# Performance work log

Hardware: AMD Instinct MI355X
Metric: run time of the kernel (lower is better)

The kernel has to match this reference:

```python
import jax, jax.numpy as jnp
import numpy as np

B, N, C = 16, 2048, 256  # dim=256, hidden_dim=2*dim -> v,gate each width C
LN_EPS = 1e-5


def setup_inputs() -> dict:
    key = jax.random.key(0)
    ks = jax.random.split(key, 6)
    std = 0.02
    return {
        "x": jax.random.normal(ks[0], (B, N, C), dtype=jnp.float32),
        "H": 64,
        "W": 32,
        "ln_w": jnp.ones((C,), jnp.float32),
        "ln_b": jnp.zeros((C,), jnp.float32),
        "w_hidden": jax.random.normal(ks[1], (C, 2 * C), jnp.float32) * std,
        "b_hidden": jnp.zeros((2 * C,), jnp.float32),
        "w_kv": jax.random.normal(ks[2], (C, C), jnp.float32) * std,  # qkv_bias=False
        "gamma": jnp.ones((2, C), jnp.float32),   # torch.ones(2, dim)
        "beta": jnp.zeros((2, C), jnp.float32),   # torch.zeros(2, dim)
        "w_proj": jax.random.normal(ks[3], (C, C), jnp.float32) * std,
        "b_proj": jnp.zeros((C,), jnp.float32),
    }


def reference(x, H, W, ln_w, ln_b, w_hidden, b_hidden, w_kv, gamma, beta, w_proj, b_proj):
    # H, W are unused by the original forward (pos conv is dead code).
    b, n, c = x.shape
    # LayerNorm
    mu = jnp.mean(x, axis=-1, keepdims=True)
    var = jnp.mean(jnp.square(x - mu), axis=-1, keepdims=True)
    normed = (x - mu) * jax.lax.rsqrt(var + LN_EPS) * ln_w + ln_b
    # to_hidden: Linear + SiLU, then chunk into v, gate (each width c)
    h = jax.nn.silu(normed @ w_hidden + b_hidden)
    v, gate = h[..., :c], h[..., c:]
    # kv projection, then offset-scale into q, k
    Z = normed @ w_kv                                  # (b, n, c)
    QK = Z[..., None, :] * gamma + beta                # (b, n, 2, c)
    q, k = QK[..., 0, :], QK[..., 1, :]
    # relu^2 quadratic attention (no softmax)
    attn = jnp.einsum('bid,bjd->bij', q, k) / n        # (b, n, n)
    A = jnp.square(jax.nn.relu(attn))
    V = jnp.einsum('bij,bjd->bid', A, v)               # (b, n, c)
    # SiLU gating, output projection, residual
    out = (V * gate) @ w_proj + b_proj
    return out + x
```

## Files before the change

### kernel.cpp

```cpp
#include <hip/hip_runtime.h>

#define BN 32768
#define NB 16
#define NN 2048
#define CC 256
#define JT 64
#define NTILES (NN / JT)

using short8  = __attribute__((ext_vector_type(8))) short;
using floatx4 = __attribute__((ext_vector_type(4))) float;

__device__ __forceinline__ unsigned short f2bf(float f) {
  unsigned u = __builtin_bit_cast(unsigned, f);
  u += 0x7fffu + ((u >> 16) & 1u);
  return (unsigned short)(u >> 16);
}
__device__ __forceinline__ float bf2f(unsigned short h) {
  unsigned u = ((unsigned)h) << 16;
  return __builtin_bit_cast(float, u);
}
__device__ __forceinline__ unsigned char f2fp8(float f) {
  return (unsigned char)(__builtin_amdgcn_cvt_pk_fp8_f32(f, f, 0, false) & 0xff);
}
__device__ __forceinline__ long lo64(uint4 v) {
  uint2 t; t.x = v.x; t.y = v.y; return __builtin_bit_cast(long, t);
}
__device__ __forceinline__ long hi64(uint4 v) {
  uint2 t; t.x = v.z; t.y = v.w; return __builtin_bit_cast(long, t);
}
__device__ __forceinline__ void gll16(const void* g, void* l) {
  __builtin_amdgcn_global_load_lds(
      (const __attribute__((address_space(1))) void*)g,
      (__attribute__((address_space(3))) void*)l, 16, 0, 0);
}

__global__ __launch_bounds__(256) void ln_kernel(
    const float* __restrict__ x, const float* __restrict__ lw,
    const float* __restrict__ lb, unsigned short* __restrict__ normed) {
  int row  = blockIdx.x * 4 + (threadIdx.x >> 6);
  int lane = threadIdx.x & 63;
  float4 v = ((const float4*)(x + (size_t)row * CC))[lane];
  float s  = v.x + v.y + v.z + v.w;
  float s2 = v.x * v.x + v.y * v.y + v.z * v.z + v.w * v.w;
#pragma unroll
  for (int off = 32; off; off >>= 1) {
    s  += __shfl_xor(s, off);
    s2 += __shfl_xor(s2, off);
  }
  float mu = s * (1.0f / CC);
  float rs = rsqrtf(s2 * (1.0f / CC) - mu * mu + 1e-5f);
  float4 w = ((const float4*)lw)[lane];
  float4 b = ((const float4*)lb)[lane];
  ushort4 o;
  o.x = f2bf((v.x - mu) * rs * w.x + b.x);
  o.y = f2bf((v.y - mu) * rs * w.y + b.y);
  o.z = f2bf((v.z - mu) * rs * w.z + b.z);
  o.w = f2bf((v.w - mu) * rs * w.w + b.w);
  ((ushort4*)(normed + (size_t)row * CC))[lane] = o;
}

__global__ void wconv_kernel(const float* __restrict__ wh,
                             const float* __restrict__ wkv,
                             const float* __restrict__ wp,
                             unsigned short* __restrict__ wTh,
                             unsigned short* __restrict__ wTkv,
                             unsigned short* __restrict__ wTp) {
  int idx = blockIdx.x * 256 + threadIdx.x;
  if (idx < 131072) {
    int n = idx >> 8, k = idx & 255;
    wTh[idx] = f2bf(wh[(size_t)k * 512 + n]);
  } else if (idx < 196608) {
    int i2 = idx - 131072;
    int n = i2 >> 8, k = i2 & 255;
    wTkv[i2] = f2bf(wkv[(size_t)k * 256 + n]);
  } else {
    int i2 = idx - 196608;
    int n = i2 >> 8, k = i2 & 255;
    wTp[i2] = f2bf(wp[(size_t)k * 256 + n]);
  }
}

__global__ __launch_bounds__(256) void gemm_hidden(
    const unsigned short* __restrict__ A, const unsigned short* __restrict__ BT,
    const float* __restrict__ bias,
    unsigned char* __restrict__ vB, unsigned short* __restrict__ gout) {
  int wave = threadIdx.x >> 6, lane = threadIdx.x & 63;
  int m = lane & 15, g4 = lane >> 4, kb = g4 * 8;
  int m0 = blockIdx.x * 128 + (wave & 1) * 64;
  int n0 = blockIdx.y * 128 + (wave >> 1) * 64;
  floatx4 acc[4][4] = {};
#pragma unroll
  for (int ks = 0; ks < 8; ++ks) {
    short8 af[4], bf[4];
#pragma unroll
    for (int i = 0; i < 4; ++i)
      af[i] = *(const short8*)(A + (size_t)(m0 + i * 16 + m) * CC + ks * 32 + kb);
#pragma unroll
    for (int j = 0; j < 4; ++j)
      bf[j] = *(const short8*)(BT + (size_t)(n0 + j * 16 + m) * CC + ks * 32 + kb);
#pragma unroll
    for (int i = 0; i < 4; ++i)
#pragma unroll
      for (int j = 0; j < 4; ++j)
        acc[i][j] = __builtin_amdgcn_mfma_f32_16x16x32_bf16(af[i], bf[j], acc[i][j], 0, 0, 0);
  }
  const size_t tb = ((size_t)(m0 >> 11) * 32 + ((m0 & 2047) >> 6)) * 16384;
#pragma unroll
  for (int j = 0; j < 4; ++j) {
    int col = n0 + j * 16 + m;
    float bv = bias[col];
    size_t colb = tb + (size_t)col * 64;
#pragma unroll
    for (int i = 0; i < 4; ++i) {
      int h8 = ((i >> 1) & 1) * 8;
      int i2 = i * 2;
#pragma unroll
      for (int r = 0; r < 4; ++r) {
        int row = m0 + i * 16 + g4 * 4 + r;
        float hh = acc[i][j][r] + bv;
        float sv = hh / (1.0f + __expf(-hh));
        if (col < CC) {
          int val = g4 * 4 + r;
          int g4a = (i2 + (val >> 3)) & 3;
          vB[colb + g4a * 16 + h8 + (val & 7)] = f2fp8(sv);
        } else {
          gout[(size_t)row * CC + col - CC] = f2bf(sv);
        }
      }
    }
  }
}

__global__ __launch_bounds__(256) void gemm_kv(
    const unsigned short* __restrict__ A, const unsigned short* __restrict__ BT,
    const float* __restrict__ gamma, const float* __restrict__ beta,
    unsigned char* __restrict__ qout, unsigned char* __restrict__ kout) {
  int wave = threadIdx.x >> 6, lane = threadIdx.x & 63;
  int m = lane & 15, g4 = lane >> 4, kb = g4 * 8;
  int m0 = blockIdx.x * 128 + (wave & 1) * 64;
  int n0 = blockIdx.y * 128 + (wave >> 1) * 64;
  floatx4 acc[4][4] = {};
#pragma unroll
  for (int ks = 0; ks < 8; ++ks) {
    short8 af[4], bf[4];
#pragma unroll
    for (int i = 0; i < 4; ++i)
      af[i] = *(const short8*)(A + (size_t)(m0 + i * 16 + m) * CC + ks * 32 + kb);
#pragma unroll
    for (int j = 0; j < 4; ++j)
      bf[j] = *(const short8*)(BT + (size_t)(n0 + j * 16 + m) * CC + ks * 32 + kb);
#pragma unroll
    for (int i = 0; i < 4; ++i)
#pragma unroll
      for (int j = 0; j < 4; ++j)
        acc[i][j] = __builtin_amdgcn_mfma_f32_16x16x32_bf16(af[i], bf[j], acc[i][j], 0, 0, 0);
  }
  const size_t base0 = ((size_t)(m0 >> 11) * 128 + ((m0 & 2047) >> 4)) * 4096;
  const int mm = g4 * 4;
#pragma unroll
  for (int j = 0; j < 4; ++j) {
    int col = n0 + j * 16 + m;
    float g0 = gamma[col], b0 = beta[col];
    float g1 = gamma[CC + col], b1 = beta[CC + col];
    int cbase = (col >> 6) * 1024 + ((col >> 3) & 3) * 16 + ((col >> 5) & 1) * 8 + (col & 7);
#pragma unroll
    for (int i = 0; i < 4; ++i) {
      size_t ibase = base0 + (size_t)i * 4096 + cbase;
#pragma unroll
      for (int r = 0; r < 4; ++r) {
        float z = acc[i][j][r];
        size_t addr = ibase + (size_t)(mm + r) * 64;
        qout[addr] = f2fp8(z * g0 + b0);
        kout[addr] = f2fp8(z * g1 + b1);
      }
    }
  }
}

__global__ __launch_bounds__(256, 2) void attn_kernel(
    const unsigned char* __restrict__ qB, const unsigned char* __restrict__ kB,
    const unsigned char* __restrict__ vB, const unsigned short* __restrict__ gg,
    unsigned short* __restrict__ og) {
  __shared__ unsigned char Kl[2][16384];
  __shared__ unsigned char Vl[2][16384];
  const int tid = threadIdx.x;
  const int wave = tid >> 6, lane = tid & 63;
  const int m = lane & 15, g4 = lane >> 4;
  const int id = blockIdx.x;
  const int b = id & 15, bx = id >> 4;
  const int i0 = bx * 64;
  const unsigned char* kimg = kB + (size_t)b * 524288;
  const unsigned char* vimg = vB + (size_t)b * 524288;

  const int iblk = bx * 4 + wave;
  uint4 qf[4];
#pragma unroll
  for (int ks2 = 0; ks2 < 4; ++ks2)
    qf[ks2] = *(const uint4*)(qB + ((size_t)(b * 128 + iblk) * 4 + ks2) * 1024 + m * 64 + g4 * 16);

  floatx4 acc[16] = {};
  const int alo = (m + ((g4 & 1) << 5)) << 2;
  const int ahi = alo + 64;

  auto stage = [&](int buf, int t) {
    const unsigned char* kt = kimg + (size_t)t * 16384;
    const unsigned char* vt = vimg + (size_t)t * 16384;
#pragma unroll
    for (int it = 0; it < 4; ++it) {
      int o = (it * 256 + tid) * 16;
      gll16(kt + o, &Kl[buf][o]);
      gll16(vt + o, &Vl[buf][o]);
    }
  };

  stage(0, 0);
  for (int t = 0; t < NTILES; ++t) {
    const int cur = t & 1;
    __syncthreads();
    if (t + 1 < NTILES) stage(cur ^ 1, t + 1);
    floatx4 sacc[4] = {};
#pragma unroll
    for (int ks2 = 0; ks2 < 4; ++ks2) {
#pragma unroll
      for (int jf = 0; jf < 4; ++jf) {
        uint4 kf = *(const uint4*)(&Kl[cur][(jf * 4 + ks2) * 1024 + m * 64 + g4 * 16]);
        sacc[jf] = __builtin_amdgcn_mfma_f32_16x16x32_fp8_fp8(
            lo64(kf), lo64(qf[ks2]), sacc[jf], 0, 0, 0);
        sacc[jf] = __builtin_amdgcn_mfma_f32_16x16x32_fp8_fp8(
            hi64(kf), hi64(qf[ks2]), sacc[jf], 0, 0, 0);
      }
    }
    unsigned pk[4];
#pragma unroll
    for (int jf = 0; jf < 4; ++jf) {
      float p0 = fmaxf(sacc[jf][0], 0.0f) * 0.0625f;
      float p1 = fmaxf(sacc[jf][1], 0.0f) * 0.0625f;
      float p2 = fmaxf(sacc[jf][2], 0.0f) * 0.0625f;
      float p3 = fmaxf(sacc[jf][3], 0.0f) * 0.0625f;
      unsigned u = __builtin_amdgcn_cvt_pk_fp8_f32(p2 * p2, p3 * p3, 0, true);
      pk[jf] = __builtin_amdgcn_cvt_pk_fp8_f32(p0 * p0, p1 * p1, (int)u, false);
    }
    long ap[2];
#pragma unroll
    for (int kk = 0; kk < 2; ++kk) {
      int A0 = __builtin_amdgcn_ds_bpermute(alo, (int)pk[2 * kk]);
      int B0 = __builtin_amdgcn_ds_bpermute(alo, (int)pk[2 * kk + 1]);
      int C0 = __builtin_amdgcn_ds_bpermute(ahi, (int)pk[2 * kk]);
      int D0 = __builtin_amdgcn_ds_bpermute(ahi, (int)pk[2 * kk + 1]);
      unsigned lo = (g4 & 2) ? (unsigned)B0 : (unsigned)A0;
      unsigned hi = (g4 & 2) ? (unsigned)D0 : (unsigned)C0;
      ap[kk] = (long)(((unsigned long long)hi << 32) | lo);
    }
#pragma unroll
    for (int cf = 0; cf < 16; ++cf) {
      uint4 vfr = *(const uint4*)(&Vl[cur][cf * 1024 + m * 64 + g4 * 16]);
      acc[cf] = __builtin_amdgcn_mfma_f32_16x16x32_fp8_fp8(ap[0], lo64(vfr), acc[cf], 0, 0, 0);
      acc[cf] = __builtin_amdgcn_mfma_f32_16x16x32_fp8_fp8(ap[1], hi64(vfr), acc[cf], 0, 0, 0);
    }
  }
  const float sc = 1.0f / 16384.0f;
  const size_t bo = (size_t)b * NN * CC;
#pragma unroll
  for (int cf = 0; cf < 16; ++cf)
#pragma unroll
    for (int r = 0; r < 4; ++r) {
      int row = i0 + wave * 16 + g4 * 4 + r;
      int col = cf * 16 + m;
      size_t off = bo + (size_t)row * CC + col;
      og[off] = f2bf(acc[cf][r] * sc * bf2f(gg[off]));
    }
}

__global__ __launch_bounds__(256) void gemm_proj(
    const unsigned short* __restrict__ A, const unsigned short* __restrict__ BT,
    const float* __restrict__ bias, const float* __restrict__ xres,
    float* __restrict__ out) {
  int wave = threadIdx.x >> 6, lane = threadIdx.x & 63;
  int m = lane & 15, g4 = lane >> 4, kb = g4 * 8;
  int m0 = blockIdx.x * 128 + (wave & 1) * 64;
  int n0 = blockIdx.y * 128 + (wave >> 1) * 64;
  floatx4 acc[4][4] = {};
#pragma unroll
  for (int ks = 0; ks < 8; ++ks) {
    short8 af[4], bf[4];
#pragma unroll
    for (int i = 0; i < 4; ++i)
      af[i] = *(const short8*)(A + (size_t)(m0 + i * 16 + m) * CC + ks * 32 + kb);
#pragma unroll
    for (int j = 0; j < 4; ++j)
      bf[j] = *(const short8*)(BT + (size_t)(n0 + j * 16 + m) * CC + ks * 32 + kb);
#pragma unroll
    for (int i = 0; i < 4; ++i)
#pragma unroll
      for (int j = 0; j < 4; ++j)
        acc[i][j] = __builtin_amdgcn_mfma_f32_16x16x32_bf16(af[i], bf[j], acc[i][j], 0, 0, 0);
  }
#pragma unroll
  for (int j = 0; j < 4; ++j) {
    int col = n0 + j * 16 + m;
    float bv = bias[col];
#pragma unroll
    for (int i = 0; i < 4; ++i)
#pragma unroll
      for (int r = 0; r < 4; ++r) {
        int row = m0 + i * 16 + g4 * 4 + r;
        size_t rr = (size_t)row * CC;
        out[rr + col] = acc[i][j][r] + bv + xres[rr + col];
      }
  }
}

extern "C" void kernel_launch(void* const* d_in, const int* in_sizes, int n_in,
                              void* d_out, int out_size, void* d_ws, size_t ws_size,
                              hipStream_t stream) {
  const float* x        = (const float*)d_in[0];
  const float* ln_w     = (const float*)d_in[3];
  const float* ln_b     = (const float*)d_in[4];
  const float* w_hidden = (const float*)d_in[5];
  const float* b_hidden = (const float*)d_in[6];
  const float* w_kv     = (const float*)d_in[7];
  const float* gamma    = (const float*)d_in[8];
  const float* beta     = (const float*)d_in[9];
  const float* w_proj   = (const float*)d_in[10];
  const float* b_proj   = (const float*)d_in[11];
  float* out = (float*)d_out;
  char* ws = (char*)d_ws;

  const size_t SZ = (size_t)BN * CC * 2;
  const size_t HZ = SZ / 2;
  unsigned short* slot0 = (unsigned short*)(ws);
  unsigned short* gbuf  = (unsigned short*)(ws + SZ);
  unsigned char*  qB    = (unsigned char*)(ws + 2 * SZ);
  unsigned char*  kB    = (unsigned char*)(ws + 2 * SZ + HZ);
  unsigned char*  vB    = (unsigned char*)(ws + 2 * SZ + 2 * HZ);
  unsigned short* wTh   = (unsigned short*)(ws + 2 * SZ + 3 * HZ);
  unsigned short* wTkv  = (unsigned short*)(ws + 2 * SZ + 3 * HZ + 512 * 256 * 2);
  unsigned short* wTp   = (unsigned short*)(ws + 2 * SZ + 3 * HZ + 512 * 256 * 2 + 256 * 256 * 2);

  wconv_kernel<<<1024, 256, 0, stream>>>(w_hidden, w_kv, w_proj, wTh, wTkv, wTp);
  ln_kernel<<<BN / 4, 256, 0, stream>>>(x, ln_w, ln_b, slot0);
  gemm_hidden<<<dim3(BN / 128, 4), 256, 0, stream>>>(slot0, wTh, b_hidden, vB, gbuf);
  gemm_kv<<<dim3(BN / 128, 2), 256, 0, stream>>>(slot0, wTkv, gamma, beta, qB, kB);
  attn_kernel<<<512, 256, 0, stream>>>(qB, kB, vB, gbuf, slot0);
  gemm_proj<<<dim3(BN / 128, 2), 256, 0, stream>>>(slot0, wTp, b_proj, x, out);
}
```

Baseline: 178.5 us.

## Swizzle K/V fp8 tile layout and pack fp8 stores in projection epilogues

```diff
diff --git a/kernel.cpp b/kernel.cpp
--- a/kernel.cpp
+++ b/kernel.cpp
@@ -21,6 +21,10 @@
 }
 __device__ __forceinline__ unsigned char f2fp8(float f) {
   return (unsigned char)(__builtin_amdgcn_cvt_pk_fp8_f32(f, f, 0, false) & 0xff);
+}
+__device__ __forceinline__ unsigned pk4fp8(float a, float b, float c, float d) {
+  unsigned u = __builtin_amdgcn_cvt_pk_fp8_f32(c, d, 0, true);
+  return __builtin_amdgcn_cvt_pk_fp8_f32(a, b, (int)u, false);
 }
 __device__ __forceinline__ long lo64(uint4 v) {
   uint2 t; t.x = v.x; t.y = v.y; return __builtin_bit_cast(long, t);
@@ -104,29 +108,43 @@
       for (int j = 0; j < 4; ++j)
         acc[i][j] = __builtin_amdgcn_mfma_f32_16x16x32_bf16(af[i], bf[j], acc[i][j], 0, 0, 0);
   }
-  const size_t tb = ((size_t)(m0 >> 11) * 32 + ((m0 & 2047) >> 6)) * 16384;
-#pragma unroll
-  for (int j = 0; j < 4; ++j) {
-    int col = n0 + j * 16 + m;
-    float bv = bias[col];
-    size_t colb = tb + (size_t)col * 64;
-#pragma unroll
-    for (int i = 0; i < 4; ++i) {
-      int h8 = ((i >> 1) & 1) * 8;
-      int i2 = i * 2;
-#pragma unroll
-      for (int r = 0; r < 4; ++r) {
-        int row = m0 + i * 16 + g4 * 4 + r;
-        float hh = acc[i][j][r] + bv;
-        float sv = hh / (1.0f + __expf(-hh));
-        if (col < CC) {
-          int val = g4 * 4 + r;
-          int g4a = (i2 + (val >> 3)) & 3;
-          vB[colb + g4a * 16 + h8 + (val & 7)] = f2fp8(sv);
-        } else {
+  const int sw = (m >> 1) & 3;
+  if (n0 < CC) {
+    const size_t tb = ((size_t)(m0 >> 11) * 32 + ((m0 & 2047) >> 6)) * 16384;
+    const int jp4 = (g4 & 1) * 4;
+    const int g4h = g4 >> 1;
+#pragma unroll
+    for (int j = 0; j < 4; ++j) {
+      int col = n0 + j * 16 + m;
+      float bv = bias[col];
+      size_t colb = tb + (size_t)col * 64;
+#pragma unroll
+      for (int i = 0; i < 4; ++i) {
+        int g4a = ((i * 2 + g4h) & 3) ^ sw;
+        int h8 = ((i >> 1) & 1) * 8;
+        float s[4];
+#pragma unroll
+        for (int r = 0; r < 4; ++r) {
+          float hh = acc[i][j][r] + bv;
+          s[r] = hh / (1.0f + __expf(-hh));
+        }
+        *(unsigned*)(vB + colb + g4a * 16 + h8 + jp4) = pk4fp8(s[0], s[1], s[2], s[3]);
+      }
+    }
+  } else {
+#pragma unroll
+    for (int j = 0; j < 4; ++j) {
+      int col = n0 + j * 16 + m;
+      float bv = bias[col];
+#pragma unroll
+      for (int i = 0; i < 4; ++i)
+#pragma unroll
+        for (int r = 0; r < 4; ++r) {
+          int row = m0 + i * 16 + g4 * 4 + r;
+          float hh = acc[i][j][r] + bv;
+          float sv = hh / (1.0f + __expf(-hh));
           gout[(size_t)row * CC + col - CC] = f2bf(sv);
         }
-      }
     }
   }
 }
@@ -153,26 +171,32 @@
     for (int i = 0; i < 4; ++i)
 #pragma unroll
       for (int j = 0; j < 4; ++j)
-        acc[i][j] = __builtin_amdgcn_mfma_f32_16x16x32_bf16(af[i], bf[j], acc[i][j], 0, 0, 0);
-  }
-  const size_t base0 = ((size_t)(m0 >> 11) * 128 + ((m0 & 2047) >> 4)) * 4096;
-  const int mm = g4 * 4;
+        acc[i][j] = __builtin_amdgcn_mfma_f32_16x16x32_bf16(bf[j], af[i], acc[i][j], 0, 0, 0);
+  }
+  const int sw = (m >> 1) & 3;
 #pragma unroll
   for (int j = 0; j < 4; ++j) {
-    int col = n0 + j * 16 + m;
-    float g0 = gamma[col], b0 = beta[col];
-    float g1 = gamma[CC + col], b1 = beta[CC + col];
-    int cbase = (col >> 6) * 1024 + ((col >> 3) & 3) * 16 + ((col >> 5) & 1) * 8 + (col & 7);
+    int c4 = n0 + j * 16 + g4 * 4;
+    float4 g0 = *(const float4*)(gamma + c4);
+    float4 b0 = *(const float4*)(beta + c4);
+    float4 g1 = *(const float4*)(gamma + CC + c4);
+    float4 b1 = *(const float4*)(beta + CC + c4);
+    int ks2 = c4 >> 6;
+    int hsub = ((c4 >> 5) & 1) * 8 + (c4 & 7);
+    int qsub = ((c4 >> 3) & 3) * 16 + hsub;
+    int ksub = ((((c4 >> 3) & 3) ^ sw)) * 16 + hsub;
 #pragma unroll
     for (int i = 0; i < 4; ++i) {
-      size_t ibase = base0 + (size_t)i * 4096 + cbase;
-#pragma unroll
-      for (int r = 0; r < 4; ++r) {
-        float z = acc[i][j][r];
-        size_t addr = ibase + (size_t)(mm + r) * 64;
-        qout[addr] = f2fp8(z * g0 + b0);
-        kout[addr] = f2fp8(z * g1 + b1);
-      }
+      int n = m0 + i * 16 + m;
+      int bb = n >> 11, jj = n & 2047;
+      size_t base = (((size_t)bb * 128 + (jj >> 4)) * 4 + ks2) * 1024 + (size_t)m * 64;
+      floatx4 z = acc[i][j];
+      unsigned qu = pk4fp8(z[0] * g0.x + b0.x, z[1] * g0.y + b0.y,
+                           z[2] * g0.z + b0.z, z[3] * g0.w + b0.w);
+      unsigned ku = pk4fp8(z[0] * g1.x + b1.x, z[1] * g1.y + b1.y,
+                           z[2] * g1.z + b1.z, z[3] * g1.w + b1.w);
+      *(unsigned*)(qout + base + qsub) = qu;
+      *(unsigned*)(kout + base + ksub) = ku;
     }
   }
 }
@@ -201,6 +225,7 @@
   floatx4 acc[16] = {};
   const int alo = (m + ((g4 & 1) << 5)) << 2;
   const int ahi = alo + 64;
+  const int gsw = (g4 ^ ((m >> 1) & 3)) * 16;
 
   auto stage = [&](int buf, int t) {
     const unsigned char* kt = kimg + (size_t)t * 16384;
@@ -223,7 +248,7 @@
     for (int ks2 = 0; ks2 < 4; ++ks2) {
 #pragma unroll
       for (int jf = 0; jf < 4; ++jf) {
-        uint4 kf = *(const uint4*)(&Kl[cur][(jf * 4 + ks2) * 1024 + m * 64 + g4 * 16]);
+        uint4 kf = *(const uint4*)(&Kl[cur][(jf * 4 + ks2) * 1024 + m * 64 + gsw]);
         sacc[jf] = __builtin_amdgcn_mfma_f32_16x16x32_fp8_fp8(
             lo64(kf), lo64(qf[ks2]), sacc[jf], 0, 0, 0);
         sacc[jf] = __builtin_amdgcn_mfma_f32_16x16x32_fp8_fp8(
@@ -237,8 +262,7 @@
       float p1 = fmaxf(sacc[jf][1], 0.0f) * 0.0625f;
       float p2 = fmaxf(sacc[jf][2], 0.0f) * 0.0625f;
       float p3 = fmaxf(sacc[jf][3], 0.0f) * 0.0625f;
-      unsigned u = __builtin_amdgcn_cvt_pk_fp8_f32(p2 * p2, p3 * p3, 0, true);
-      pk[jf] = __builtin_amdgcn_cvt_pk_fp8_f32(p0 * p0, p1 * p1, (int)u, false);
+      pk[jf] = pk4fp8(p0 * p0, p1 * p1, p2 * p2, p3 * p3);
     }
     long ap[2];
 #pragma unroll
@@ -253,7 +277,7 @@
     }
 #pragma unroll
     for (int cf = 0; cf < 16; ++cf) {
-      uint4 vfr = *(const uint4*)(&Vl[cur][cf * 1024 + m * 64 + g4 * 16]);
+      uint4 vfr = *(const uint4*)(&Vl[cur][cf * 1024 + m * 64 + gsw]);
       acc[cf] = __builtin_amdgcn_mfma_f32_16x16x32_fp8_fp8(ap[0], lo64(vfr), acc[cf], 0, 0, 0);
       acc[cf] = __builtin_amdgcn_mfma_f32_16x16x32_fp8_fp8(ap[1], hi64(vfr), acc[cf], 0, 0, 0);
     }
```

Result: faster. 166.7 us (-6.6%).
